# Performance work log

Hardware: AMD Instinct MI355X
Metric: run time of the kernel (lower is better)

## Reference

```python
import jax, jax.numpy as jnp
import numpy as np

N_NODES = 100000
N_EDGES = 1600000
DIM_IN = 128
DIM_OUT = 128


def setup_inputs() -> dict:
    key = jax.random.key(0)
    k1, k2, k3 = jax.random.split(key, 3)
    x = jax.random.normal(k1, (N_NODES, DIM_IN), dtype=jnp.float32)
    W = jax.random.normal(k2, (DIM_OUT, DIM_IN), dtype=jnp.float32) * (1.0 / np.sqrt(DIM_IN))
    bias = jnp.zeros((DIM_OUT,), dtype=jnp.float32)
    edge_index = jax.random.randint(k3, (2, N_EDGES), 0, N_NODES, dtype=jnp.int64)
    return {"x": x, "W": W, "bias": bias, "edge_index": edge_index}


def reference(x, W, bias, edge_index):
    N = x.shape[0]
    # add self loops
    loops = jnp.arange(N, dtype=edge_index.dtype)
    row = jnp.concatenate([edge_index[0], loops])  # source nodes (x_j)
    col = jnp.concatenate([edge_index[1], loops])  # target nodes (aggregation)
    # linear transform (no bias inside lin)
    h = x @ W.T  # [N, out]
    # symmetric degree normalization, degree computed over col incl. self loops
    deg = jax.ops.segment_sum(jnp.ones_like(col, dtype=x.dtype), col, num_segments=N)
    deg_inv_sqrt = jnp.where(deg > 0, deg ** -0.5, 0.0)
    norm = deg_inv_sqrt[row] * deg_inv_sqrt[col]  # [E+N]
    # gather-scale-scatter_add
    msg = norm[:, None] * h[row]  # [E+N, out]
    out = jax.ops.segment_sum(msg, col, num_segments=N)
    return out + bias
```

## Files before the change

kernel.cpp:

```cpp
#include <hip/hip_runtime.h>

#define DIM 128
#define CAP 64
#define BUCKET_BLOCKS 1024
#define GEMM_BLOCKS 1568
#define GRID_COMBO (BUCKET_BLOCKS + GEMM_BLOCKS)


typedef __attribute__((ext_vector_type(8))) short bf16x8;
typedef __attribute__((ext_vector_type(4))) float f32x4;

__device__ __forceinline__ unsigned short f2bf(float f) {
  unsigned int u = __float_as_uint(f);
  return (unsigned short)((u + 0x7FFFu + ((u >> 16) & 1u)) >> 16);
}
__device__ __forceinline__ float bf2f(unsigned int s) {
  return __uint_as_float(s << 16);
}

__global__ __launch_bounds__(256) void prep_kernel(
    const float* __restrict__ W, unsigned short* __restrict__ Wb,
    int* __restrict__ cnt, int N) {
  int i = blockIdx.x * 256 + threadIdx.x;
  if (i < DIM * DIM) Wb[i] = f2bf(W[i]);
  if (i < N) cnt[i] = 0;
}

__global__ __launch_bounds__(256) void combo_kernel(
    const int* __restrict__ rows, const int* __restrict__ cols,
    int* __restrict__ cnt, int* __restrict__ csr,
    const float* __restrict__ x, const unsigned short* __restrict__ Wb,
    unsigned short* __restrict__ h, int E, int N) {
  if (blockIdx.x < BUCKET_BLOCKS) {
    int bid = blockIdx.x;
    int g = bid & 7;
    int gblk = bid >> 3;
    int lo = (int)((long long)g * N / 8);
    int hi = (int)((long long)(g + 1) * N / 8);
    const int4* cols4 = (const int4*)cols;
    int E4 = E >> 2;
    for (int i = gblk * 256 + threadIdx.x; i < E4;
         i += (BUCKET_BLOCKS / 8) * 256) {
      int4 c4 = cols4[i];
      int e = i * 4;
      if (c4.x >= lo && c4.x < hi) {
        int k = atomicAdd(&cnt[c4.x], 1);
        if (k < CAP) csr[(size_t)c4.x * CAP + k] = rows[e];
      }
      if (c4.y >= lo && c4.y < hi) {
        int k = atomicAdd(&cnt[c4.y], 1);
        if (k < CAP) csr[(size_t)c4.y * CAP + k] = rows[e + 1];
      }
      if (c4.z >= lo && c4.z < hi) {
        int k = atomicAdd(&cnt[c4.z], 1);
        if (k < CAP) csr[(size_t)c4.z * CAP + k] = rows[e + 2];
      }
      if (c4.w >= lo && c4.w < hi) {
        int k = atomicAdd(&cnt[c4.w], 1);
        if (k < CAP) csr[(size_t)c4.w * CAP + k] = rows[e + 3];
      }
    }
    if (gblk == 0) {
      for (int e = (E & ~3) + threadIdx.x; e < E; e += 256) {
        int c = cols[e];
        if (c >= lo && c < hi) {
          int k = atomicAdd(&cnt[c], 1);
          if (k < CAP) csr[(size_t)c * CAP + k] = rows[e];
        }
      }
    }
  } else {
    int wid = (blockIdx.x - BUCKET_BLOCKS) * 4 + (threadIdx.x >> 6);
    int m0 = wid * 16;
    if (m0 >= N) return;
    int lane = threadIdx.x & 63;
    int mr = lane & 15;
    int quad = lane >> 4;

    bf16x8 afrag[4];
    const float* xrow = x + (size_t)(m0 + mr) * DIM + quad * 8;
#pragma unroll
    for (int ks = 0; ks < 4; ++ks) {
      float4 lo = *(const float4*)(xrow + ks * 32);
      float4 hi = *(const float4*)(xrow + ks * 32 + 4);
      bf16x8 a;
      a[0] = (short)f2bf(lo.x); a[1] = (short)f2bf(lo.y);
      a[2] = (short)f2bf(lo.z); a[3] = (short)f2bf(lo.w);
      a[4] = (short)f2bf(hi.x); a[5] = (short)f2bf(hi.y);
      a[6] = (short)f2bf(hi.z); a[7] = (short)f2bf(hi.w);
      afrag[ks] = a;
    }

#pragma unroll
    for (int nt = 0; nt < 8; ++nt) {
      f32x4 c = {0.f, 0.f, 0.f, 0.f};
#pragma unroll
      for (int ks = 0; ks < 4; ++ks) {
        bf16x8 b = *(const bf16x8*)(Wb + (size_t)(nt * 16 + mr) * DIM +
                                    ks * 32 + quad * 8);
        c = __builtin_amdgcn_mfma_f32_16x16x32_bf16(afrag[ks], b, c, 0, 0, 0);
      }
#pragma unroll
      for (int r = 0; r < 4; ++r) {
        h[(size_t)(m0 + quad * 4 + r) * DIM + nt * 16 + mr] = f2bf(c[r]);
      }
    }
  }
}

__global__ __launch_bounds__(256) void gather_kernel(
    const uint4* __restrict__ h4, const int* __restrict__ csr,
    const int* __restrict__ cnt, const float4* __restrict__ bias4,
    float4* __restrict__ out4, int N) {
  int node = blockIdx.x * 16 + (threadIdx.x >> 4);
  if (node >= N) return;
  int lane = threadIdx.x & 15;

  int degN = cnt[node];
  float dn = rsqrtf((float)degN + 1.0f);
  int deg = degN > CAP ? CAP : degN;
  const int* seg = csr + (size_t)node * CAP;

  float acc[8];
  {
    uint4 s = h4[(size_t)node * 16 + lane];
    acc[0] = dn * bf2f(s.x & 0xFFFF); acc[1] = dn * bf2f(s.x >> 16);
    acc[2] = dn * bf2f(s.y & 0xFFFF); acc[3] = dn * bf2f(s.y >> 16);
    acc[4] = dn * bf2f(s.z & 0xFFFF); acc[5] = dn * bf2f(s.z >> 16);
    acc[6] = dn * bf2f(s.w & 0xFFFF); acc[7] = dn * bf2f(s.w >> 16);
  }
  for (int j = 0; j < deg; ++j) {
    int r = seg[j];
    float dr = rsqrtf((float)cnt[r] + 1.0f);
    uint4 v = h4[(size_t)r * 16 + lane];
    acc[0] += dr * bf2f(v.x & 0xFFFF); acc[1] += dr * bf2f(v.x >> 16);
    acc[2] += dr * bf2f(v.y & 0xFFFF); acc[3] += dr * bf2f(v.y >> 16);
    acc[4] += dr * bf2f(v.z & 0xFFFF); acc[5] += dr * bf2f(v.z >> 16);
    acc[6] += dr * bf2f(v.w & 0xFFFF); acc[7] += dr * bf2f(v.w >> 16);
  }
  float4 bA = bias4[lane * 2], bB = bias4[lane * 2 + 1];
  float4 oA = {dn * acc[0] + bA.x, dn * acc[1] + bA.y,
               dn * acc[2] + bA.z, dn * acc[3] + bA.w};
  float4 oB = {dn * acc[4] + bB.x, dn * acc[5] + bB.y,
               dn * acc[6] + bB.z, dn * acc[7] + bB.w};
  out4[(size_t)node * 32 + lane * 2]     = oA;
  out4[(size_t)node * 32 + lane * 2 + 1] = oB;
}

extern "C" void kernel_launch(void* const* d_in, const int* in_sizes, int n_in,
                              void* d_out, int out_size, void* d_ws, size_t ws_size,
                              hipStream_t stream) {
  const float* x    = (const float*)d_in[0];
  const float* W    = (const float*)d_in[1];
  const float* bias = (const float*)d_in[2];
  const int*   ei   = (const int*)d_in[3];

  const int N = in_sizes[0] / DIM;
  const int E = in_sizes[3] / 2;
  const int* rows = ei;
  const int* cols = ei + E;
  float* out = (float*)d_out;
  char* ws = (char*)d_ws;

  int* cnt = (int*)ws;
  unsigned short* Wb = (unsigned short*)(ws + 409600);
  int* csr = (int*)(ws + 442368);
  unsigned short* h = (unsigned short*)(ws + 26042368);

  prep_kernel<<<(N + 255) / 256, 256, 0, stream>>>(W, Wb, cnt, N);
  combo_kernel<<<GRID_COMBO, 256, 0, stream>>>(rows, cols, cnt, csr, x, Wb, h,
                                               E, N);
  gather_kernel<<<(N + 15) / 16, 256, 0, stream>>>(
      (const uint4*)h, csr, cnt, (const float4*)bias, (float4*)out, N);
}
```

Before: 274.4 us.

## Split combined bucket/GEMM kernel, add nontemporal loads, unroll gather by two

Splits the fused bucket+GEMM kernel into two separate launches and doubles the bucket grid. The bucket pass now uses nontemporal vector loads of cols and only loads the rows vector when one of its four edges falls in the block's node range. The gather loop is unrolled by two to issue more independent neighbour loads, and output stores are nontemporal. The split gives up the overlap between bucketing and GEMM and adds one extra launch, in exchange for simpler kernels and less redundant row traffic.

```diff
diff --git a/kernel.cpp b/kernel.cpp
--- a/kernel.cpp
+++ b/kernel.cpp
@@ -2,13 +2,13 @@
 
 #define DIM 128
 #define CAP 64
-#define BUCKET_BLOCKS 1024
-#define GEMM_BLOCKS 1568
-#define GRID_COMBO (BUCKET_BLOCKS + GEMM_BLOCKS)
+#define BUCKET_BLOCKS 2048
+#define GEMM_BLOCKS 1563
 
 
 typedef __attribute__((ext_vector_type(8))) short bf16x8;
 typedef __attribute__((ext_vector_type(4))) float f32x4;
+typedef __attribute__((ext_vector_type(4))) int i32x4;
 
 __device__ __forceinline__ unsigned short f2bf(float f) {
   unsigned int u = __float_as_uint(f);
@@ -26,84 +26,91 @@
   if (i < N) cnt[i] = 0;
 }
 
-__global__ __launch_bounds__(256) void combo_kernel(
+__global__ __launch_bounds__(256) void bucket_kernel(
     const int* __restrict__ rows, const int* __restrict__ cols,
-    int* __restrict__ cnt, int* __restrict__ csr,
+    int* __restrict__ cnt, int* __restrict__ csr, int E, int N) {
+  int bid = blockIdx.x;
+  int g = bid & 7;
+  int gblk = bid >> 3;
+  int lo = (int)((long long)g * N / 8);
+  int hi = (int)((long long)(g + 1) * N / 8);
+  const i32x4* cols4 = (const i32x4*)cols;
+  const i32x4* rows4 = (const i32x4*)rows;
+  int E4 = E >> 2;
+  for (int i = gblk * 256 + threadIdx.x; i < E4;
+       i += (BUCKET_BLOCKS / 8) * 256) {
+    i32x4 c4 = __builtin_nontemporal_load(&cols4[i]);
+    bool mx = (c4.x >= lo) & (c4.x < hi);
+    bool my = (c4.y >= lo) & (c4.y < hi);
+    bool mz = (c4.z >= lo) & (c4.z < hi);
+    bool mw = (c4.w >= lo) & (c4.w < hi);
+    if (mx | my | mz | mw) {
+      i32x4 r4 = __builtin_nontemporal_load(&rows4[i]);
+      if (mx) {
+        int k = atomicAdd(&cnt[c4.x], 1);
+        if (k < CAP) csr[(size_t)c4.x * CAP + k] = r4.x;
+      }
+      if (my) {
+        int k = atomicAdd(&cnt[c4.y], 1);
+        if (k < CAP) csr[(size_t)c4.y * CAP + k] = r4.y;
+      }
+      if (mz) {
+        int k = atomicAdd(&cnt[c4.z], 1);
+        if (k < CAP) csr[(size_t)c4.z * CAP + k] = r4.z;
+      }
+      if (mw) {
+        int k = atomicAdd(&cnt[c4.w], 1);
+        if (k < CAP) csr[(size_t)c4.w * CAP + k] = r4.w;
+      }
+    }
+  }
+  if (bid < 8 && gblk == 0) {
+    for (int e = (E & ~3) + threadIdx.x; e < E; e += 256) {
+      int c = cols[e];
+      if (c >= lo && c < hi) {
+        int k = atomicAdd(&cnt[c], 1);
+        if (k < CAP) csr[(size_t)c * CAP + k] = rows[e];
+      }
+    }
+  }
+}
+
+__global__ __launch_bounds__(256) void gemm_kernel(
     const float* __restrict__ x, const unsigned short* __restrict__ Wb,
-    unsigned short* __restrict__ h, int E, int N) {
-  if (blockIdx.x < BUCKET_BLOCKS) {
-    int bid = blockIdx.x;
-    int g = bid & 7;
-    int gblk = bid >> 3;
-    int lo = (int)((long long)g * N / 8);
-    int hi = (int)((long long)(g + 1) * N / 8);
-    const int4* cols4 = (const int4*)cols;
-    int E4 = E >> 2;
-    for (int i = gblk * 256 + threadIdx.x; i < E4;
-         i += (BUCKET_BLOCKS / 8) * 256) {
-      int4 c4 = cols4[i];
-      int e = i * 4;
-      if (c4.x >= lo && c4.x < hi) {
-        int k = atomicAdd(&cnt[c4.x], 1);
-        if (k < CAP) csr[(size_t)c4.x * CAP + k] = rows[e];
-      }
-      if (c4.y >= lo && c4.y < hi) {
-        int k = atomicAdd(&cnt[c4.y], 1);
-        if (k < CAP) csr[(size_t)c4.y * CAP + k] = rows[e + 1];
-      }
-      if (c4.z >= lo && c4.z < hi) {
-        int k = atomicAdd(&cnt[c4.z], 1);
-        if (k < CAP) csr[(size_t)c4.z * CAP + k] = rows[e + 2];
-      }
-      if (c4.w >= lo && c4.w < hi) {
-        int k = atomicAdd(&cnt[c4.w], 1);
-        if (k < CAP) csr[(size_t)c4.w * CAP + k] = rows[e + 3];
-      }
-    }
-    if (gblk == 0) {
-      for (int e = (E & ~3) + threadIdx.x; e < E; e += 256) {
-        int c = cols[e];
-        if (c >= lo && c < hi) {
-          int k = atomicAdd(&cnt[c], 1);
-          if (k < CAP) csr[(size_t)c * CAP + k] = rows[e];
-        }
-      }
-    }
-  } else {
-    int wid = (blockIdx.x - BUCKET_BLOCKS) * 4 + (threadIdx.x >> 6);
-    int m0 = wid * 16;
-    if (m0 >= N) return;
-    int lane = threadIdx.x & 63;
-    int mr = lane & 15;
-    int quad = lane >> 4;
-
-    bf16x8 afrag[4];
-    const float* xrow = x + (size_t)(m0 + mr) * DIM + quad * 8;
+    unsigned short* __restrict__ h, int N) {
+  int wid = blockIdx.x * 4 + (threadIdx.x >> 6);
+  int m0 = wid * 16;
+  if (m0 >= N) return;
+  int lane = threadIdx.x & 63;
+  int mr = lane & 15;
+  int quad = lane >> 4;
+
+  bf16x8 afrag[4];
+  const float* xrow = x + (size_t)(m0 + mr) * DIM + quad * 8;
+#pragma unroll
+  for (int ks = 0; ks < 4; ++ks) {
+    f32x4 lo = __builtin_nontemporal_load((const f32x4*)(xrow + ks * 32));
+    f32x4 hi = __builtin_nontemporal_load((const f32x4*)(xrow + ks * 32 + 4));
+    bf16x8 a;
+    a[0] = (short)f2bf(lo.x); a[1] = (short)f2bf(lo.y);
+    a[2] = (short)f2bf(lo.z); a[3] = (short)f2bf(lo.w);
+    a[4] = (short)f2bf(hi.x); a[5] = (short)f2bf(hi.y);
+    a[6] = (short)f2bf(hi.z); a[7] = (short)f2bf(hi.w);
+    afrag[ks] = a;
+  }
+
+#pragma unroll
+  for (int nt = 0; nt < 8; ++nt) {
+    f32x4 c = {0.f, 0.f, 0.f, 0.f};
 #pragma unroll
     for (int ks = 0; ks < 4; ++ks) {
-      float4 lo = *(const float4*)(xrow + ks * 32);
-      float4 hi = *(const float4*)(xrow + ks * 32 + 4);
-      bf16x8 a;
-      a[0] = (short)f2bf(lo.x); a[1] = (short)f2bf(lo.y);
-      a[2] = (short)f2bf(lo.z); a[3] = (short)f2bf(lo.w);
-      a[4] = (short)f2bf(hi.x); a[5] = (short)f2bf(hi.y);
-      a[6] = (short)f2bf(hi.z); a[7] = (short)f2bf(hi.w);
-      afrag[ks] = a;
-    }
-
-#pragma unroll
-    for (int nt = 0; nt < 8; ++nt) {
-      f32x4 c = {0.f, 0.f, 0.f, 0.f};
-#pragma unroll
-      for (int ks = 0; ks < 4; ++ks) {
-        bf16x8 b = *(const bf16x8*)(Wb + (size_t)(nt * 16 + mr) * DIM +
-                                    ks * 32 + quad * 8);
-        c = __builtin_amdgcn_mfma_f32_16x16x32_bf16(afrag[ks], b, c, 0, 0, 0);
-      }
-#pragma unroll
-      for (int r = 0; r < 4; ++r) {
-        h[(size_t)(m0 + quad * 4 + r) * DIM + nt * 16 + mr] = f2bf(c[r]);
-      }
+      bf16x8 b = *(const bf16x8*)(Wb + (size_t)(nt * 16 + mr) * DIM +
+                                  ks * 32 + quad * 8);
+      c = __builtin_amdgcn_mfma_f32_16x16x32_bf16(afrag[ks], b, c, 0, 0, 0);
+    }
+#pragma unroll
+    for (int r = 0; r < 4; ++r) {
+      h[(size_t)(m0 + quad * 4 + r) * DIM + nt * 16 + mr] = f2bf(c[r]);
     }
   }
 }
@@ -111,7 +118,7 @@
 __global__ __launch_bounds__(256) void gather_kernel(
     const uint4* __restrict__ h4, const int* __restrict__ csr,
     const int* __restrict__ cnt, const float4* __restrict__ bias4,
-    float4* __restrict__ out4, int N) {
+    float* __restrict__ out, int N) {
   int node = blockIdx.x * 16 + (threadIdx.x >> 4);
   if (node >= N) return;
   int lane = threadIdx.x & 15;
@@ -129,22 +136,40 @@
     acc[4] = dn * bf2f(s.z & 0xFFFF); acc[5] = dn * bf2f(s.z >> 16);
     acc[6] = dn * bf2f(s.w & 0xFFFF); acc[7] = dn * bf2f(s.w >> 16);
   }
-  for (int j = 0; j < deg; ++j) {
-    int r = seg[j];
+  int j = 0;
+  for (; j + 2 <= deg; j += 2) {
+    int r0 = __builtin_nontemporal_load(seg + j);
+    int r1 = __builtin_nontemporal_load(seg + j + 1);
+    uint4 v0 = h4[(size_t)r0 * 16 + lane];
+    uint4 v1 = h4[(size_t)r1 * 16 + lane];
+    float dr0 = rsqrtf((float)cnt[r0] + 1.0f);
+    float dr1 = rsqrtf((float)cnt[r1] + 1.0f);
+    acc[0] += dr0 * bf2f(v0.x & 0xFFFF); acc[1] += dr0 * bf2f(v0.x >> 16);
+    acc[2] += dr0 * bf2f(v0.y & 0xFFFF); acc[3] += dr0 * bf2f(v0.y >> 16);
+    acc[4] += dr0 * bf2f(v0.z & 0xFFFF); acc[5] += dr0 * bf2f(v0.z >> 16);
+    acc[6] += dr0 * bf2f(v0.w & 0xFFFF); acc[7] += dr0 * bf2f(v0.w >> 16);
+    acc[0] += dr1 * bf2f(v1.x & 0xFFFF); acc[1] += dr1 * bf2f(v1.x >> 16);
+    acc[2] += dr1 * bf2f(v1.y & 0xFFFF); acc[3] += dr1 * bf2f(v1.y >> 16);
+    acc[4] += dr1 * bf2f(v1.z & 0xFFFF); acc[5] += dr1 * bf2f(v1.z >> 16);
+    acc[6] += dr1 * bf2f(v1.w & 0xFFFF); acc[7] += dr1 * bf2f(v1.w >> 16);
+  }
+  if (j < deg) {
+    int r = __builtin_nontemporal_load(seg + j);
+    uint4 v = h4[(size_t)r * 16 + lane];
     float dr = rsqrtf((float)cnt[r] + 1.0f);
-    uint4 v = h4[(size_t)r * 16 + lane];
     acc[0] += dr * bf2f(v.x & 0xFFFF); acc[1] += dr * bf2f(v.x >> 16);
     acc[2] += dr * bf2f(v.y & 0xFFFF); acc[3] += dr * bf2f(v.y >> 16);
     acc[4] += dr * bf2f(v.z & 0xFFFF); acc[5] += dr * bf2f(v.z >> 16);
     acc[6] += dr * bf2f(v.w & 0xFFFF); acc[7] += dr * bf2f(v.w >> 16);
   }
   float4 bA = bias4[lane * 2], bB = bias4[lane * 2 + 1];
-  float4 oA = {dn * acc[0] + bA.x, dn * acc[1] + bA.y,
-               dn * acc[2] + bA.z, dn * acc[3] + bA.w};
-  float4 oB = {dn * acc[4] + bB.x, dn * acc[5] + bB.y,
-               dn * acc[6] + bB.z, dn * acc[7] + bB.w};
-  out4[(size_t)node * 32 + lane * 2]     = oA;
-  out4[(size_t)node * 32 + lane * 2 + 1] = oB;
+  f32x4 oA = {dn * acc[0] + bA.x, dn * acc[1] + bA.y,
+              dn * acc[2] + bA.z, dn * acc[3] + bA.w};
+  f32x4 oB = {dn * acc[4] + bB.x, dn * acc[5] + bB.y,
+              dn * acc[6] + bB.z, dn * acc[7] + bB.w};
+  f32x4* outv = (f32x4*)out;
+  __builtin_nontemporal_store(oA, &outv[(size_t)node * 32 + lane * 2]);
+  __builtin_nontemporal_store(oB, &outv[(size_t)node * 32 + lane * 2 + 1]);
 }
 
 extern "C" void kernel_launch(void* const* d_in, const int* in_sizes, int n_in,
@@ -168,8 +193,8 @@
   unsigned short* h = (unsigned short*)(ws + 26042368);
 
   prep_kernel<<<(N + 255) / 256, 256, 0, stream>>>(W, Wb, cnt, N);
-  combo_kernel<<<GRID_COMBO, 256, 0, stream>>>(rows, cols, cnt, csr, x, Wb, h,
-                                               E, N);
+  bucket_kernel<<<BUCKET_BLOCKS, 256, 0, stream>>>(rows, cols, cnt, csr, E, N);
+  gemm_kernel<<<GEMM_BLOCKS, 256, 0, stream>>>(x, Wb, h, N);
   gather_kernel<<<(N + 15) / 16, 256, 0, stream>>>(
-      (const uint4*)h, csr, cnt, (const float4*)bias, (float4*)out, N);
-}
+      (const uint4*)h, csr, cnt, (const float4*)bias, out, N);
+}
```

Result: slower. 287.6 us (+4.8%).
